# Optimization experiments

Hardware: AMD Instinct MI355X
Metric: run time of the kernel (lower is better)

The kernel has to match this reference:

```python
import jax, jax.numpy as jnp
import numpy as np

B, L, D = 8, 256, 256  # batch, max sentence length, channel_in == channel_out


def setup_inputs() -> dict:
    key = jax.random.key(0)
    k1, k2, k3, k4, k5, k6 = jax.random.split(key, 6)
    queries = jax.random.normal(k1, (B, L, D), dtype=jnp.float32)
    wordlens = jax.random.randint(k2, (B,), 1, L, dtype=jnp.int32)
    syntactic_dep = jax.random.randint(k3, (B, L, L), 0, 2, dtype=jnp.int32)
    # w_wc[0]: Linear(2D -> D, no bias); split its weight into the h_i and h_j halves.
    s1 = 1.0 / np.sqrt(2 * D)
    Wa = jax.random.normal(k4, (D, D), dtype=jnp.float32) * s1
    Wb = jax.random.normal(jax.random.fold_in(k4, 1), (D, D), dtype=jnp.float32) * s1
    # w_wc[3]: Linear(D -> 1, no bias)
    w2 = jax.random.normal(k5, (D,), dtype=jnp.float32) * (1.0 / np.sqrt(D))
    # wd: Linear(D -> D, no bias)
    Wd = jax.random.normal(k6, (D, D), dtype=jnp.float32) * (1.0 / np.sqrt(D))
    return {"queries": queries, "wordlens": wordlens, "syntactic_dep": syntactic_dep,
            "Wa": Wa, "Wb": Wb, "w2": w2, "Wd": Wd}


def reference(queries, wordlens, syntactic_dep, Wa, Wb, w2, Wd):
    # queries: [B, L, D]; syntactic_dep: [B, L, L] (nonzero => edge i->j)
    mask = syntactic_dep > 0
    # Edge score t_ij = w2 . relu(Wa h_i + Wb h_j)  (dropout is identity at eval)
    A = jnp.einsum('bid,cd->bic', queries, Wa)   # [B, L, C]
    Bm = jnp.einsum('bjd,cd->bjc', queries, Wb)  # [B, L, C]
    pre = jax.nn.relu(A[:, :, None, :] + Bm[:, None, :, :])  # [B, L, L, C]
    t = jnp.einsum('bijc,c->bij', pre, w2)       # [B, L, L]
    # T initialized to -100 everywhere, edge positions get t (exactly as original)
    T = jnp.where(mask, t, jnp.float32(-100.0))
    beta = jax.nn.softmax(T, axis=-1)            # softmax over j (dim=1 of [L, L])
    w = beta * mask.astype(beta.dtype)           # zero out non-edges after softmax
    hj = jnp.einsum('bjd,cd->bjc', queries, Wd)  # wd(h_j), [B, L, C]
    agg = jnp.einsum('bij,bjc->bic', w, hj)      # weighted neighbor sum
    output = jax.nn.relu(queries + agg)
    # skip=False, so no extra residual add
    return (output, wordlens, syntactic_dep)
```

## Files before the change

kernel.cpp:

```cpp
#include <hip/hip_runtime.h>

#define NB 8
#define LL 256
#define DD 256

typedef __attribute__((ext_vector_type(8))) short short8v;
typedef __attribute__((ext_vector_type(4))) float f32x4;
typedef __attribute__((ext_vector_type(2))) float f32x2;

#if defined(__has_builtin)
#if __has_builtin(__builtin_elementwise_fma) && __has_builtin(__builtin_elementwise_max)
#define USE_PK 1
#endif
#endif

__device__ __forceinline__ uint f2bf2(float lo, float hi) {
  uint a = __float_as_uint(lo), b = __float_as_uint(hi);
  uint ra = (a + 0x7FFFu + ((a >> 16) & 1u)) >> 16;
  uint rb = (b + 0x7FFFu + ((b >> 16) & 1u)) & 0xFFFF0000u;
  return ra | rb;
}

__global__ __launch_bounds__(256, 3) void gemm3_mfma(
    const float* __restrict__ Q, const float* __restrict__ Wa,
    const float* __restrict__ Wb, const float* __restrict__ Wd,
    const int* __restrict__ wl, const int* __restrict__ sdep,
    float* __restrict__ A, float* __restrict__ Bm, float* __restrict__ Hj,
    float* __restrict__ tail) {
  const int mt = blockIdx.x, nt = blockIdx.y, z = blockIdx.z;
  const int bid = mt + 32 * (nt + 8 * z);
  const float* __restrict__ W = (z == 0) ? Wa : (z == 1) ? Wb : Wd;
  float* __restrict__ Out = (z == 0) ? A : (z == 1) ? Bm : Hj;

  __shared__ __align__(16) ushort Qs[64][32];
  __shared__ __align__(16) ushort Ws[32][32];

  const int tid = threadIdx.x;
  const int m0 = mt * 64, n0 = nt * 32;
  const int srow = tid >> 2, skc = (tid & 3) * 8;
  const int w = tid >> 6, lane = tid & 63;
  const int wm = w >> 1, wn = w & 1;
  const int fr = lane & 15, fk = (lane >> 4) * 8;

  f32x4 acc[2] = {};
  for (int k0 = 0; k0 < DD; k0 += 32) {
    {
      const float* src = &Q[(size_t)(m0 + srow) * DD + k0 + skc];
      float4 q0 = *(const float4*)src;
      float4 q1 = *(const float4*)(src + 4);
      uint4 pk = make_uint4(f2bf2(q0.x, q0.y), f2bf2(q0.z, q0.w),
                            f2bf2(q1.x, q1.y), f2bf2(q1.z, q1.w));
      *(uint4*)&Qs[srow][skc] = pk;
    }
    if (tid < 128) {
      const float* ws_ = &W[(size_t)(n0 + srow) * DD + k0 + skc];
      float4 w0 = *(const float4*)ws_;
      float4 w1 = *(const float4*)(ws_ + 4);
      uint4 pw = make_uint4(f2bf2(w0.x, w0.y), f2bf2(w0.z, w0.w),
                            f2bf2(w1.x, w1.y), f2bf2(w1.z, w1.w));
      *(uint4*)&Ws[srow][skc] = pw;
    }
    __syncthreads();
    short8v a0 = *(const short8v*)&Qs[wm * 32 + fr][fk];
    short8v a1 = *(const short8v*)&Qs[wm * 32 + 16 + fr][fk];
    short8v b0 = *(const short8v*)&Ws[wn * 16 + fr][fk];
    acc[0] = __builtin_amdgcn_mfma_f32_16x16x32_bf16(a0, b0, acc[0], 0, 0, 0);
    acc[1] = __builtin_amdgcn_mfma_f32_16x16x32_bf16(a1, b0, acc[1], 0, 0, 0);
    __syncthreads();
  }

  const int rbase = m0 + wm * 32 + (lane >> 4) * 4;
  const int cbase = n0 + wn * 16 + fr;
#pragma unroll
  for (int i = 0; i < 2; ++i)
#pragma unroll
    for (int r = 0; r < 4; ++r)
      Out[(size_t)(rbase + i * 16 + r) * DD + cbase] = acc[i][r];

  {
    int t = bid * 256 + tid;
    if (t < 131072) {
      int4 s = *(const int4*)&sdep[(size_t)t * 4];
      float4 f;
      f.x = (float)s.x; f.y = (float)s.y; f.z = (float)s.z; f.w = (float)s.w;
      *(float4*)&tail[8 + (size_t)t * 4] = f;
    }
  }
  if (bid == 0 && tid < 8) tail[tid] = (float)wl[tid];
}

__global__ __launch_bounds__(512, 2) void fused_kernel(
    const float* __restrict__ Q, const int* __restrict__ sdep,
    const float* __restrict__ w2, const float* __restrict__ A,
    const float* __restrict__ Bm, const float* __restrict__ Hj,
    float* __restrict__ out) {
  const int bid = blockIdx.x;
  const int b = bid & 7, it = bid >> 3;
  const int i0 = it * 8;
  const int tid = threadIdx.x;
  const int w = tid >> 6, l = tid & 63;
  const int j0 = w * 32;

  __shared__ float Ts[8][260];
  __shared__ float Red[8][4][256];

  {
    const int jp = l >> 4;
    const int cg = l & 15;
    f32x2 a2[8][8], wv2[8];
    const float* Ab = A + ((size_t)(b * LL + i0)) * DD + cg * 16;
#pragma unroll
    for (int r = 0; r < 8; ++r)
#pragma unroll
      for (int ch = 0; ch < 4; ++ch) {
        float4 t = *(const float4*)&Ab[(size_t)r * DD + ch * 4];
        a2[r][ch * 2] = (f32x2){t.x, t.y};
        a2[r][ch * 2 + 1] = (f32x2){t.z, t.w};
      }
#pragma unroll
    for (int ch = 0; ch < 4; ++ch) {
      float4 t = *(const float4*)&w2[cg * 16 + ch * 4];
      wv2[ch * 2] = (f32x2){t.x, t.y};
      wv2[ch * 2 + 1] = (f32x2){t.z, t.w};
    }

    const float* Bb = Bm + ((size_t)(b * LL + j0 + jp)) * DD + cg * 16;
#pragma unroll 2
    for (int s = 0; s < 8; ++s) {
      f32x2 bv2[8];
#pragma unroll
      for (int ch = 0; ch < 4; ++ch) {
        float4 t = *(const float4*)&Bb[(size_t)(s * 4) * DD + ch * 4];
        bv2[ch * 2] = (f32x2){t.x, t.y};
        bv2[ch * 2 + 1] = (f32x2){t.z, t.w};
      }
      f32x2 p2[8] = {};
#pragma unroll
      for (int u = 0; u < 8; ++u) {
        f32x2 bb = bv2[u], ww = wv2[u];
#pragma unroll
        for (int r = 0; r < 8; ++r) {
#ifdef USE_PK
          f32x2 sm = __builtin_elementwise_max(a2[r][u] + bb, (f32x2){0.f, 0.f});
          p2[r] = __builtin_elementwise_fma(ww, sm, p2[r]);
#else
          f32x2 t0 = a2[r][u] + bb;
          f32x2 sm = {fmaxf(t0.x, 0.f), fmaxf(t0.y, 0.f)};
          p2[r].x = fmaf(ww.x, sm.x, p2[r].x);
          p2[r].y = fmaf(ww.y, sm.y, p2[r].y);
#endif
        }
      }
      float p0 = p2[0].x + p2[0].y, p1 = p2[1].x + p2[1].y;
      float p2s = p2[2].x + p2[2].y, p3 = p2[3].x + p2[3].y;
      float p4 = p2[4].x + p2[4].y, p5 = p2[5].x + p2[5].y;
      float p6 = p2[6].x + p2[6].y, p7 = p2[7].x + p2[7].y;
#pragma unroll
      for (int m = 1; m <= 8; m <<= 1) {
        p0 += __shfl_xor(p0, m); p1 += __shfl_xor(p1, m);
        p2s += __shfl_xor(p2s, m); p3 += __shfl_xor(p3, m);
        p4 += __shfl_xor(p4, m); p5 += __shfl_xor(p5, m);
        p6 += __shfl_xor(p6, m); p7 += __shfl_xor(p7, m);
      }
      float pv = p0;
      pv = (cg == 1) ? p1 : pv; pv = (cg == 2) ? p2s : pv;
      pv = (cg == 3) ? p3 : pv; pv = (cg == 4) ? p4 : pv;
      pv = (cg == 5) ? p5 : pv; pv = (cg == 6) ? p6 : pv;
      pv = (cg == 7) ? p7 : pv;
      if (cg < 8) Ts[cg][j0 + s * 4 + jp] = pv;
    }
  }
  __syncthreads();

  {
    const int* sr = sdep + ((size_t)(b * LL + i0 + w)) * LL;
    float v[4];
    float m = -3.0e38f;
#pragma unroll
    for (int k = 0; k < 4; ++k) {
      int j = l + 64 * k;
      bool e = sr[j] > 0;
      v[k] = e ? Ts[w][j] : -3.0e38f;
      m = fmaxf(m, v[k]);
    }
#pragma unroll
    for (int off = 32; off >= 1; off >>= 1) m = fmaxf(m, __shfl_xor(m, off));
    float s = 0.f;
#pragma unroll
    for (int k = 0; k < 4; ++k) {
      float e = (v[k] > -1.0e30f) ? __expf(v[k] - m) : 0.f;
      v[k] = e;
      s += e;
    }
#pragma unroll
    for (int off = 32; off >= 1; off >>= 1) s += __shfl_xor(s, off);
    float inv = (s > 0.f) ? 1.0f / s : 0.f;
    __syncthreads();
#pragma unroll
    for (int k = 0; k < 4; ++k) Ts[w][l + 64 * k] = v[k] * inv;
  }
  __syncthreads();

  const float* Hb = Hj + ((size_t)(b * LL + j0)) * DD + l * 4;
#pragma unroll
  for (int g = 0; g < 2; ++g) {
    {
      float acc[4][4] = {};
#pragma unroll 2
      for (int j4 = 0; j4 < 8; ++j4) {
        float tw0[4], tw1[4], tw2[4], tw3[4];
        *(float4*)tw0 = *(const float4*)&Ts[g * 4 + 0][j0 + j4 * 4];
        *(float4*)tw1 = *(const float4*)&Ts[g * 4 + 1][j0 + j4 * 4];
        *(float4*)tw2 = *(const float4*)&Ts[g * 4 + 2][j0 + j4 * 4];
        *(float4*)tw3 = *(const float4*)&Ts[g * 4 + 3][j0 + j4 * 4];
#pragma unroll
        for (int u = 0; u < 4; ++u) {
          float4 h = *(const float4*)&Hb[(size_t)(j4 * 4 + u) * DD];
          acc[0][0] = fmaf(tw0[u], h.x, acc[0][0]);
          acc[0][1] = fmaf(tw0[u], h.y, acc[0][1]);
          acc[0][2] = fmaf(tw0[u], h.z, acc[0][2]);
          acc[0][3] = fmaf(tw0[u], h.w, acc[0][3]);
          acc[1][0] = fmaf(tw1[u], h.x, acc[1][0]);
          acc[1][1] = fmaf(tw1[u], h.y, acc[1][1]);
          acc[1][2] = fmaf(tw1[u], h.z, acc[1][2]);
          acc[1][3] = fmaf(tw1[u], h.w, acc[1][3]);
          acc[2][0] = fmaf(tw2[u], h.x, acc[2][0]);
          acc[2][1] = fmaf(tw2[u], h.y, acc[2][1]);
          acc[2][2] = fmaf(tw2[u], h.z, acc[2][2]);
          acc[2][3] = fmaf(tw2[u], h.w, acc[2][3]);
          acc[3][0] = fmaf(tw3[u], h.x, acc[3][0]);
          acc[3][1] = fmaf(tw3[u], h.y, acc[3][1]);
          acc[3][2] = fmaf(tw3[u], h.z, acc[3][2]);
          acc[3][3] = fmaf(tw3[u], h.w, acc[3][3]);
        }
      }
#pragma unroll
      for (int r = 0; r < 4; ++r)
        *(float4*)&Red[w][r][l * 4] = *(float4*)acc[r];
    }
    __syncthreads();
    if (tid < 256) {
      const int r = tid >> 6, q = tid & 63;
      float4 s0 = *(const float4*)&Red[0][r][q * 4];
      float4 s1 = *(const float4*)&Red[1][r][q * 4];
      float4 s2 = *(const float4*)&Red[2][r][q * 4];
      float4 s3 = *(const float4*)&Red[3][r][q * 4];
      float4 s4 = *(const float4*)&Red[4][r][q * 4];
      float4 s5 = *(const float4*)&Red[5][r][q * 4];
      float4 s6 = *(const float4*)&Red[6][r][q * 4];
      float4 s7 = *(const float4*)&Red[7][r][q * 4];
      size_t off = ((size_t)(b * LL + i0 + g * 4 + r)) * DD + q * 4;
      float4 qv = *(const float4*)&Q[off];
      float4 o;
      o.x = fmaxf(qv.x + ((s0.x + s1.x) + (s2.x + s3.x)) +
                          ((s4.x + s5.x) + (s6.x + s7.x)), 0.f);
      o.y = fmaxf(qv.y + ((s0.y + s1.y) + (s2.y + s3.y)) +
                          ((s4.y + s5.y) + (s6.y + s7.y)), 0.f);
      o.z = fmaxf(qv.z + ((s0.z + s1.z) + (s2.z + s3.z)) +
                          ((s4.z + s5.z) + (s6.z + s7.z)), 0.f);
      o.w = fmaxf(qv.w + ((s0.w + s1.w) + (s2.w + s3.w)) +
                          ((s4.w + s5.w) + (s6.w + s7.w)), 0.f);
      *(float4*)&out[off] = o;
    }
    __syncthreads();
  }
}

extern "C" void kernel_launch(void* const* d_in, const int* in_sizes, int n_in,
                              void* d_out, int out_size, void* d_ws, size_t ws_size,
                              hipStream_t stream) {
  const float* Q    = (const float*)d_in[0];
  const int*   wl   = (const int*)d_in[1];
  const int*   sdep = (const int*)d_in[2];
  const float* Wa   = (const float*)d_in[3];
  const float* Wb   = (const float*)d_in[4];
  const float* w2   = (const float*)d_in[5];
  const float* Wd   = (const float*)d_in[6];
  float* out = (float*)d_out;
  float* ws  = (float*)d_ws;

  float* A  = ws;
  float* Bm = ws + 524288;
  float* Hj = ws + 1048576;
  float* tail = out + (size_t)NB * LL * DD;

  gemm3_mfma<<<dim3(32, 8, 3), 256, 0, stream>>>(Q, Wa, Wb, Wd, wl, sdep,
                                                 A, Bm, Hj, tail);
  fused_kernel<<<256, 512, 0, stream>>>(Q, sdep, w2, A, Bm, Hj, out);
}
```

Baseline: 100.7 us.

## Shrink fused kernel blocks to four rows and 256 threads, doubling grid

Each block of the fused score/softmax/aggregation kernel now handles 4 query rows instead of 8, with 4 waves each covering 64 columns, and the grid doubles to 512 blocks. The per-thread accumulator state in the score loop is halved, which lowers register pressure and may allow more waves per CU. An unneeded barrier and the two-pass output loop are removed. In exchange, the B and Hj tiles are reused across fewer rows per block, which increases global/L2 traffic.

```diff
diff --git a/kernel.cpp b/kernel.cpp
--- a/kernel.cpp
+++ b/kernel.cpp
@@ -89,28 +89,28 @@
   if (bid == 0 && tid < 8) tail[tid] = (float)wl[tid];
 }
 
-__global__ __launch_bounds__(512, 2) void fused_kernel(
+__global__ __launch_bounds__(256) void fused_kernel(
     const float* __restrict__ Q, const int* __restrict__ sdep,
     const float* __restrict__ w2, const float* __restrict__ A,
     const float* __restrict__ Bm, const float* __restrict__ Hj,
     float* __restrict__ out) {
   const int bid = blockIdx.x;
   const int b = bid & 7, it = bid >> 3;
-  const int i0 = it * 8;
+  const int i0 = it * 4;
   const int tid = threadIdx.x;
   const int w = tid >> 6, l = tid & 63;
-  const int j0 = w * 32;
-
-  __shared__ float Ts[8][260];
-  __shared__ float Red[8][4][256];
+  const int j0 = w * 64;
+
+  __shared__ float Ts[4][260];
+  __shared__ float Red[4][4][256];
 
   {
     const int jp = l >> 4;
     const int cg = l & 15;
-    f32x2 a2[8][8], wv2[8];
+    f32x2 a2[4][8], wv2[8];
     const float* Ab = A + ((size_t)(b * LL + i0)) * DD + cg * 16;
 #pragma unroll
-    for (int r = 0; r < 8; ++r)
+    for (int r = 0; r < 4; ++r)
 #pragma unroll
       for (int ch = 0; ch < 4; ++ch) {
         float4 t = *(const float4*)&Ab[(size_t)r * DD + ch * 4];
@@ -125,8 +125,8 @@
     }
 
     const float* Bb = Bm + ((size_t)(b * LL + j0 + jp)) * DD + cg * 16;
-#pragma unroll 2
-    for (int s = 0; s < 8; ++s) {
+#pragma unroll 4
+    for (int s = 0; s < 16; ++s) {
       f32x2 bv2[8];
 #pragma unroll
       for (int ch = 0; ch < 4; ++ch) {
@@ -134,12 +134,12 @@
         bv2[ch * 2] = (f32x2){t.x, t.y};
         bv2[ch * 2 + 1] = (f32x2){t.z, t.w};
       }
-      f32x2 p2[8] = {};
+      f32x2 p2[4] = {};
 #pragma unroll
       for (int u = 0; u < 8; ++u) {
         f32x2 bb = bv2[u], ww = wv2[u];
 #pragma unroll
-        for (int r = 0; r < 8; ++r) {
+        for (int r = 0; r < 4; ++r) {
 #ifdef USE_PK
           f32x2 sm = __builtin_elementwise_max(a2[r][u] + bb, (f32x2){0.f, 0.f});
           p2[r] = __builtin_elementwise_fma(ww, sm, p2[r]);
@@ -152,22 +152,17 @@
         }
       }
       float p0 = p2[0].x + p2[0].y, p1 = p2[1].x + p2[1].y;
-      float p2s = p2[2].x + p2[2].y, p3 = p2[3].x + p2[3].y;
-      float p4 = p2[4].x + p2[4].y, p5 = p2[5].x + p2[5].y;
-      float p6 = p2[6].x + p2[6].y, p7 = p2[7].x + p2[7].y;
+      float q2 = p2[2].x + p2[2].y, p3 = p2[3].x + p2[3].y;
 #pragma unroll
       for (int m = 1; m <= 8; m <<= 1) {
         p0 += __shfl_xor(p0, m); p1 += __shfl_xor(p1, m);
-        p2s += __shfl_xor(p2s, m); p3 += __shfl_xor(p3, m);
-        p4 += __shfl_xor(p4, m); p5 += __shfl_xor(p5, m);
-        p6 += __shfl_xor(p6, m); p7 += __shfl_xor(p7, m);
+        q2 += __shfl_xor(q2, m); p3 += __shfl_xor(p3, m);
       }
       float pv = p0;
-      pv = (cg == 1) ? p1 : pv; pv = (cg == 2) ? p2s : pv;
-      pv = (cg == 3) ? p3 : pv; pv = (cg == 4) ? p4 : pv;
-      pv = (cg == 5) ? p5 : pv; pv = (cg == 6) ? p6 : pv;
-      pv = (cg == 7) ? p7 : pv;
-      if (cg < 8) Ts[cg][j0 + s * 4 + jp] = pv;
+      pv = (cg == 1) ? p1 : pv;
+      pv = (cg == 2) ? q2 : pv;
+      pv = (cg == 3) ? p3 : pv;
+      if (cg < 4) Ts[cg][j0 + s * 4 + jp] = pv;
     }
   }
   __syncthreads();
@@ -195,74 +190,62 @@
 #pragma unroll
     for (int off = 32; off >= 1; off >>= 1) s += __shfl_xor(s, off);
     float inv = (s > 0.f) ? 1.0f / s : 0.f;
-    __syncthreads();
 #pragma unroll
     for (int k = 0; k < 4; ++k) Ts[w][l + 64 * k] = v[k] * inv;
   }
   __syncthreads();
 
-  const float* Hb = Hj + ((size_t)(b * LL + j0)) * DD + l * 4;
-#pragma unroll
-  for (int g = 0; g < 2; ++g) {
-    {
-      float acc[4][4] = {};
+  {
+    const float* Hb = Hj + ((size_t)(b * LL + j0)) * DD + l * 4;
+    float acc[4][4] = {};
 #pragma unroll 2
-      for (int j4 = 0; j4 < 8; ++j4) {
-        float tw0[4], tw1[4], tw2[4], tw3[4];
-        *(float4*)tw0 = *(const float4*)&Ts[g * 4 + 0][j0 + j4 * 4];
-        *(float4*)tw1 = *(const float4*)&Ts[g * 4 + 1][j0 + j4 * 4];
-        *(float4*)tw2 = *(const float4*)&Ts[g * 4 + 2][j0 + j4 * 4];
-        *(float4*)tw3 = *(const float4*)&Ts[g * 4 + 3][j0 + j4 * 4];
-#pragma unroll
-        for (int u = 0; u < 4; ++u) {
-          float4 h = *(const float4*)&Hb[(size_t)(j4 * 4 + u) * DD];
-          acc[0][0] = fmaf(tw0[u], h.x, acc[0][0]);
-          acc[0][1] = fmaf(tw0[u], h.y, acc[0][1]);
-          acc[0][2] = fmaf(tw0[u], h.z, acc[0][2]);
-          acc[0][3] = fmaf(tw0[u], h.w, acc[0][3]);
-          acc[1][0] = fmaf(tw1[u], h.x, acc[1][0]);
-          acc[1][1] = fmaf(tw1[u], h.y, acc[1][1]);
-          acc[1][2] = fmaf(tw1[u], h.z, acc[1][2]);
-          acc[1][3] = fmaf(tw1[u], h.w, acc[1][3]);
-          acc[2][0] = fmaf(tw2[u], h.x, acc[2][0]);
-          acc[2][1] = fmaf(tw2[u], h.y, acc[2][1]);
-          acc[2][2] = fmaf(tw2[u], h.z, acc[2][2]);
-          acc[2][3] = fmaf(tw2[u], h.w, acc[2][3]);
-          acc[3][0] = fmaf(tw3[u], h.x, acc[3][0]);
-          acc[3][1] = fmaf(tw3[u], h.y, acc[3][1]);
-          acc[3][2] = fmaf(tw3[u], h.z, acc[3][2]);
-          acc[3][3] = fmaf(tw3[u], h.w, acc[3][3]);
-        }
-      }
-#pragma unroll
-      for (int r = 0; r < 4; ++r)
-        *(float4*)&Red[w][r][l * 4] = *(float4*)acc[r];
-    }
-    __syncthreads();
-    if (tid < 256) {
-      const int r = tid >> 6, q = tid & 63;
-      float4 s0 = *(const float4*)&Red[0][r][q * 4];
-      float4 s1 = *(const float4*)&Red[1][r][q * 4];
-      float4 s2 = *(const float4*)&Red[2][r][q * 4];
-      float4 s3 = *(const float4*)&Red[3][r][q * 4];
-      float4 s4 = *(const float4*)&Red[4][r][q * 4];
-      float4 s5 = *(const float4*)&Red[5][r][q * 4];
-      float4 s6 = *(const float4*)&Red[6][r][q * 4];
-      float4 s7 = *(const float4*)&Red[7][r][q * 4];
-      size_t off = ((size_t)(b * LL + i0 + g * 4 + r)) * DD + q * 4;
-      float4 qv = *(const float4*)&Q[off];
-      float4 o;
-      o.x = fmaxf(qv.x + ((s0.x + s1.x) + (s2.x + s3.x)) +
-                          ((s4.x + s5.x) + (s6.x + s7.x)), 0.f);
-      o.y = fmaxf(qv.y + ((s0.y + s1.y) + (s2.y + s3.y)) +
-                          ((s4.y + s5.y) + (s6.y + s7.y)), 0.f);
-      o.z = fmaxf(qv.z + ((s0.z + s1.z) + (s2.z + s3.z)) +
-                          ((s4.z + s5.z) + (s6.z + s7.z)), 0.f);
-      o.w = fmaxf(qv.w + ((s0.w + s1.w) + (s2.w + s3.w)) +
-                          ((s4.w + s5.w) + (s6.w + s7.w)), 0.f);
-      *(float4*)&out[off] = o;
-    }
-    __syncthreads();
+    for (int j4 = 0; j4 < 16; ++j4) {
+      float tw0[4], tw1[4], tw2[4], tw3[4];
+      *(float4*)tw0 = *(const float4*)&Ts[0][j0 + j4 * 4];
+      *(float4*)tw1 = *(const float4*)&Ts[1][j0 + j4 * 4];
+      *(float4*)tw2 = *(const float4*)&Ts[2][j0 + j4 * 4];
+      *(float4*)tw3 = *(const float4*)&Ts[3][j0 + j4 * 4];
+#pragma unroll
+      for (int u = 0; u < 4; ++u) {
+        float4 h = *(const float4*)&Hb[(size_t)(j4 * 4 + u) * DD];
+        acc[0][0] = fmaf(tw0[u], h.x, acc[0][0]);
+        acc[0][1] = fmaf(tw0[u], h.y, acc[0][1]);
+        acc[0][2] = fmaf(tw0[u], h.z, acc[0][2]);
+        acc[0][3] = fmaf(tw0[u], h.w, acc[0][3]);
+        acc[1][0] = fmaf(tw1[u], h.x, acc[1][0]);
+        acc[1][1] = fmaf(tw1[u], h.y, acc[1][1]);
+        acc[1][2] = fmaf(tw1[u], h.z, acc[1][2]);
+        acc[1][3] = fmaf(tw1[u], h.w, acc[1][3]);
+        acc[2][0] = fmaf(tw2[u], h.x, acc[2][0]);
+        acc[2][1] = fmaf(tw2[u], h.y, acc[2][1]);
+        acc[2][2] = fmaf(tw2[u], h.z, acc[2][2]);
+        acc[2][3] = fmaf(tw2[u], h.w, acc[2][3]);
+        acc[3][0] = fmaf(tw3[u], h.x, acc[3][0]);
+        acc[3][1] = fmaf(tw3[u], h.y, acc[3][1]);
+        acc[3][2] = fmaf(tw3[u], h.z, acc[3][2]);
+        acc[3][3] = fmaf(tw3[u], h.w, acc[3][3]);
+      }
+    }
+#pragma unroll
+    for (int r = 0; r < 4; ++r)
+      *(float4*)&Red[w][r][l * 4] = *(float4*)acc[r];
+  }
+  __syncthreads();
+
+  {
+    const int r = tid >> 6, q = tid & 63;
+    float4 s0 = *(const float4*)&Red[0][r][q * 4];
+    float4 s1 = *(const float4*)&Red[1][r][q * 4];
+    float4 s2 = *(const float4*)&Red[2][r][q * 4];
+    float4 s3 = *(const float4*)&Red[3][r][q * 4];
+    size_t off = ((size_t)(b * LL + i0 + r)) * DD + q * 4;
+    float4 qv = *(const float4*)&Q[off];
+    float4 o;
+    o.x = fmaxf(qv.x + (s0.x + s1.x) + (s2.x + s3.x), 0.f);
+    o.y = fmaxf(qv.y + (s0.y + s1.y) + (s2.y + s3.y), 0.f);
+    o.z = fmaxf(qv.z + (s0.z + s1.z) + (s2.z + s3.z), 0.f);
+    o.w = fmaxf(qv.w + (s0.w + s1.w) + (s2.w + s3.w), 0.f);
+    *(float4*)&out[off] = o;
   }
 }
 
@@ -286,5 +269,5 @@
 
   gemm3_mfma<<<dim3(32, 8, 3), 256, 0, stream>>>(Q, Wa, Wb, Wd, wl, sdep,
                                                  A, Bm, Hj, tail);
-  fused_kernel<<<256, 512, 0, stream>>>(Q, sdep, w2, A, Bm, Hj, out);
-}
+  fused_kernel<<<512, 256, 0, stream>>>(Q, sdep, w2, A, Bm, Hj, out);
+}
```

New measurement: 101.7 us. About the same (+1.0%).
